# Optimization experiments

Hardware: AMD Instinct MI355X
Metric: run time of the kernel (lower is better)

## Reference

```python
import jax, jax.numpy as jnp
import numpy as np

B, L, I, O = 65536, 16, 256, 256


def setup_inputs() -> dict:
    key = jax.random.key(0)
    k1, k2, k3, k4 = jax.random.split(key, 4)
    lookups = jax.random.uniform(k1, (B, L), dtype=jnp.float32)
    values = jax.random.normal(k2, (B, I), dtype=jnp.float32)
    # glorot-style scale for the weight bank
    weights_lookup = jax.random.normal(k3, (L, I, O), dtype=jnp.float32) * (1.0 / np.sqrt(I))
    bias_lookup = jnp.zeros((L, O), dtype=jnp.float32)
    return {"lookups": lookups, "values": values,
            "weights_lookup": weights_lookup, "bias_lookup": bias_lookup}


def reference(lookups, values, weights_lookup, bias_lookup):
    # tf.einsum('...i,...l,lio->...o') with bias einsum('...l,lo->...o'),
    # activation = 'linear' (identity).
    # Efficient contraction order: per-token routed values (b,l,i) is avoided by
    # contracting values with the weight bank per expert, then combining with
    # routing weights — equivalent math, single einsum lets XLA pick the order.
    weighted = jnp.einsum('bi,bl,lio->bo', values, lookups, weights_lookup)
    biases = jnp.einsum('bl,lo->bo', lookups, bias_lookup)
    return weighted + biases
```

## Files before the change

kernel.cpp:

```cpp
#include <hip/hip_runtime.h>
#include <hip/hip_fp16.h>
#include <stdint.h>


#define B_TOK 65536
#define L_DIM 16
#define I_DIM 256
#define O_DIM 256
#define NKT   65
#define BM    256
#define BN    256
#define BK    64
#define THREADS 512

typedef __attribute__((ext_vector_type(8))) _Float16 f16x8;
typedef __attribute__((ext_vector_type(4))) float f32x4;

typedef __attribute__((address_space(3))) void      lds_void_t;
typedef const __attribute__((address_space(1))) void gbl_void_t;

__global__ void prep_w(const float* __restrict__ W, const float* __restrict__ bias,
                       unsigned short* __restrict__ ws) {
    const int t = blockIdx.x;
    const int o = threadIdx.x;
    char* dstRow = (char*)(ws + (size_t)t * 16384) + o * 128;
    if (t < 64) {
        const int l = t & 15, ibase = (t >> 4) * 64;
        const float* src = W + ((size_t)l * I_DIM + ibase) * O_DIM + o;
#pragma unroll
        for (int c = 0; c < 8; ++c) {
            uint32_t p[4];
#pragma unroll
            for (int jp = 0; jp < 4; ++jp) {
                float a = src[(size_t)(c * 8 + 2 * jp) * O_DIM];
                float b = src[(size_t)(c * 8 + 2 * jp + 1) * O_DIM];
                p[jp] = __builtin_bit_cast(uint32_t, __floats2half2_rn(a, b));
            }
            uint4 q = {p[0], p[1], p[2], p[3]};
            *(uint4*)(dstRow + ((c ^ (o & 7)) * 16)) = q;
        }
    } else {
#pragma unroll
        for (int c = 0; c < 8; ++c) {
            uint32_t p[4] = {0u, 0u, 0u, 0u};
            if (c < 2) {
#pragma unroll
                for (int jp = 0; jp < 4; ++jp) {
                    int kk = c * 8 + 2 * jp;
                    float a = bias[(size_t)kk * O_DIM + o];
                    float b = bias[(size_t)(kk + 1) * O_DIM + o];
                    p[jp] = __builtin_bit_cast(uint32_t, __floats2half2_rn(a, b));
                }
            }
            uint4 q = {p[0], p[1], p[2], p[3]};
            *(uint4*)(dstRow + ((c ^ (o & 7)) * 16)) = q;
        }
    }
}

__launch_bounds__(THREADS, 2)
__global__ void md_gemm(const float* __restrict__ lookups,
                        const float* __restrict__ values,
                        const unsigned short* __restrict__ Wst,
                        float* __restrict__ out) {
    __shared__ char smem[2 * 65536];

    const int tid  = threadIdx.x;
    const int wid  = tid >> 6;
    const int lane = tid & 63;
    const int row0 = blockIdx.x * BM;

    const int r = tid >> 1;
    const int h = tid & 1;

    const int wm   = wid >> 2;
    const int wn   = wid & 3;
    const int arow = wm * 128 + (lane & 15);
    const int bcol = wn * 64  + (lane & 15);
    const int kkl  = (lane >> 4) * 8;

    f32x4 acc[8][4];
#pragma unroll
    for (int m = 0; m < 8; ++m)
#pragma unroll
        for (int n = 0; n < 4; ++n) acc[m][n] = (f32x4){0.f, 0.f, 0.f, 0.f};

    __half2 hvv[16];

    auto stageB = [&](int kt, int nb) {
        const char* src = (const char*)Wst + (size_t)kt * 32768 + wid * 1024 + lane * 16;
        char* dst = smem + nb * 65536 + 32768 + wid * 1024;
#pragma unroll
        for (int s = 0; s < 4; ++s)
            __builtin_amdgcn_global_load_lds((gbl_void_t*)(src + s * 8192),
                                             (lds_void_t*)(dst + s * 8192), 16, 0, 0);
    };

    auto prepA = [&](int kt) {
        if (kt < 64) {
            if ((kt & 15) == 0) {
                const float4* vp = (const float4*)(values + (size_t)(row0 + r) * I_DIM
                                                   + (kt >> 4) * 64 + h * 32);
#pragma unroll
                for (int j = 0; j < 8; ++j) {
                    float4 f = vp[j];
                    hvv[2 * j]     = __floats2half2_rn(f.x, f.y);
                    hvv[2 * j + 1] = __floats2half2_rn(f.z, f.w);
                }
            }
        } else {
            if (h == 0) {
                const float4* lp = (const float4*)(lookups + (size_t)(row0 + r) * L_DIM);
#pragma unroll
                for (int j = 0; j < 4; ++j) {
                    float4 f = lp[j];
                    hvv[2 * j]     = __floats2half2_rn(f.x, f.y);
                    hvv[2 * j + 1] = __floats2half2_rn(f.z, f.w);
                }
#pragma unroll
                for (int j = 8; j < 16; ++j) hvv[j] = __floats2half2_rn(0.f, 0.f);
            } else {
#pragma unroll
                for (int j = 0; j < 16; ++j) hvv[j] = __floats2half2_rn(0.f, 0.f);
            }
        }
    };

    auto writeA = [&](int nb, float sc) {
        __half2 s2 = __float2half2_rn(sc);
        uint32_t p[16];
#pragma unroll
        for (int i = 0; i < 16; ++i)
            p[i] = __builtin_bit_cast(uint32_t, __hmul2(hvv[i], s2));
        char* abase = smem + nb * 65536;
#pragma unroll
        for (int w = 0; w < 4; ++w) {
            uint4 q = {p[4 * w], p[4 * w + 1], p[4 * w + 2], p[4 * w + 3]};
            *(uint4*)(abase + ((r * 128 + h * 64 + w * 16) ^ ((r & 7) << 4))) = q;
        }
    };

    auto compute = [&](int bs) {
        char* abase = smem + bs * 65536;
        char* bbase = abase + 32768;
#pragma unroll
        for (int ks = 0; ks < 2; ++ks) {
            const int kk2 = kkl * 2 + ks * 64;
            f16x8 af[8], bfr[4];
#pragma unroll
            for (int nt = 0; nt < 4; ++nt) {
                int o = bcol + nt * 16;
                bfr[nt] = *(f16x8*)(bbase + ((o * 128 + kk2) ^ ((o & 7) << 4)));
            }
#pragma unroll
            for (int mt = 0; mt < 8; ++mt) {
                int row = arow + mt * 16;
                af[mt] = *(f16x8*)(abase + ((row * 128 + kk2) ^ ((row & 7) << 4)));
            }
#pragma unroll
            for (int mt = 0; mt < 8; ++mt)
#pragma unroll
                for (int nt = 0; nt < 4; ++nt)
                    acc[mt][nt] = __builtin_amdgcn_mfma_f32_16x16x32_f16(
                        af[mt], bfr[nt], acc[mt][nt], 0, 0, 0);
        }
    };

    stageB(0, 0);
    prepA(0);
    {
        float lk0 = lookups[(size_t)(row0 + r) * L_DIM];
        writeA(0, lk0);
    }
    __syncthreads();

    int bsel = 0;
    for (int kt = 0; kt < NKT; ++kt) {
        float lkn = 0.f;
        if (kt + 1 < NKT) {
            stageB(kt + 1, bsel ^ 1);
            prepA(kt + 1);
            lkn = (kt + 1 < 64) ? lookups[(size_t)(row0 + r) * L_DIM + ((kt + 1) & 15)]
                                : 1.0f;
        }
        compute(bsel);
        if (kt + 1 < NKT) writeA(bsel ^ 1, lkn);
        __syncthreads();
        bsel ^= 1;
    }

    const int orow = row0 + wm * 128 + (lane >> 4) * 4;
    const int ocol = wn * 64 + (lane & 15);
#pragma unroll
    for (int mt = 0; mt < 8; ++mt)
#pragma unroll
        for (int nt = 0; nt < 4; ++nt) {
#pragma unroll
            for (int j = 0; j < 4; ++j)
                out[(size_t)(orow + mt * 16 + j) * O_DIM + ocol + nt * 16] = acc[mt][nt][j];
        }
}

extern "C" void kernel_launch(void* const* d_in, const int* in_sizes, int n_in,
                              void* d_out, int out_size, void* d_ws, size_t ws_size,
                              hipStream_t stream) {
    const float* lookups = (const float*)d_in[0];
    const float* values  = (const float*)d_in[1];
    const float* W       = (const float*)d_in[2];
    const float* bias    = (const float*)d_in[3];
    unsigned short* Wst  = (unsigned short*)d_ws;

    prep_w<<<dim3(NKT), dim3(256), 0, stream>>>(W, bias, Wst);
    md_gemm<<<dim3(B_TOK / BM), dim3(THREADS), 0, stream>>>(lookups, values, Wst,
                                                            (float*)d_out);
}
```

Baseline: 231.7 us.

## Keep values tile resident per chunk and scale by lookups in registers

The A (values) tile is now written to LDS once per 64-wide input chunk and reused across all 16 experts. Each expert's routing weight is applied to the A fragments in registers, with the lookups read from an LDS cache, instead of rewriting the scaled A tile to LDS on every k-step. B staging uses a separate double buffer synchronised with a raw waitcnt plus barrier, and the bias tile is handled as a final step. prep_w is also spread over more blocks so the weight conversion runs with more parallelism. The intent is to cut LDS writes, global lookup loads and sync overhead, at the cost of more hand-written synchronisation that could hide races.

```diff
diff --git a/kernel.cpp b/kernel.cpp
--- a/kernel.cpp
+++ b/kernel.cpp
@@ -7,55 +7,54 @@
 #define L_DIM 16
 #define I_DIM 256
 #define O_DIM 256
-#define NKT   65
 #define BM    256
-#define BN    256
-#define BK    64
 #define THREADS 512
+
+#define AOFF  65536
+#define LKOFF 98304
+#define LKS   20
 
 typedef __attribute__((ext_vector_type(8))) _Float16 f16x8;
 typedef __attribute__((ext_vector_type(4))) float f32x4;
-
 typedef __attribute__((address_space(3))) void      lds_void_t;
 typedef const __attribute__((address_space(1))) void gbl_void_t;
 
+static __device__ __forceinline__ f16x8 scale8(f16x8 a, __half2 s) {
+    union { f16x8 v; __half2 h[4]; } u; u.v = a;
+#pragma unroll
+    for (int q = 0; q < 4; ++q) u.h[q] = __hmul2(u.h[q], s);
+    return u.v;
+}
+
 __global__ void prep_w(const float* __restrict__ W, const float* __restrict__ bias,
                        unsigned short* __restrict__ ws) {
-    const int t = blockIdx.x;
-    const int o = threadIdx.x;
-    char* dstRow = (char*)(ws + (size_t)t * 16384) + o * 128;
+    const int t  = blockIdx.x;
+    const int o  = blockIdx.y * 32 + (threadIdx.x & 31);
+    const int cp = threadIdx.x >> 5;
+    const int c  = cp ^ (o & 7);
+    uint32_t p[4];
     if (t < 64) {
         const int l = t & 15, ibase = (t >> 4) * 64;
-        const float* src = W + ((size_t)l * I_DIM + ibase) * O_DIM + o;
-#pragma unroll
-        for (int c = 0; c < 8; ++c) {
-            uint32_t p[4];
-#pragma unroll
-            for (int jp = 0; jp < 4; ++jp) {
-                float a = src[(size_t)(c * 8 + 2 * jp) * O_DIM];
-                float b = src[(size_t)(c * 8 + 2 * jp + 1) * O_DIM];
-                p[jp] = __builtin_bit_cast(uint32_t, __floats2half2_rn(a, b));
-            }
-            uint4 q = {p[0], p[1], p[2], p[3]};
-            *(uint4*)(dstRow + ((c ^ (o & 7)) * 16)) = q;
+        const float* src = W + ((size_t)l * I_DIM + ibase + c * 8) * O_DIM + o;
+#pragma unroll
+        for (int jp = 0; jp < 4; ++jp) {
+            float a = src[(size_t)(2 * jp) * O_DIM];
+            float b = src[(size_t)(2 * jp + 1) * O_DIM];
+            p[jp] = __builtin_bit_cast(uint32_t, __floats2half2_rn(a, b));
+        }
+    } else if (c < 2) {
+#pragma unroll
+        for (int jp = 0; jp < 4; ++jp) {
+            int kk = c * 8 + 2 * jp;
+            float a = bias[(size_t)kk * O_DIM + o];
+            float b = bias[(size_t)(kk + 1) * O_DIM + o];
+            p[jp] = __builtin_bit_cast(uint32_t, __floats2half2_rn(a, b));
         }
     } else {
-#pragma unroll
-        for (int c = 0; c < 8; ++c) {
-            uint32_t p[4] = {0u, 0u, 0u, 0u};
-            if (c < 2) {
-#pragma unroll
-                for (int jp = 0; jp < 4; ++jp) {
-                    int kk = c * 8 + 2 * jp;
-                    float a = bias[(size_t)kk * O_DIM + o];
-                    float b = bias[(size_t)(kk + 1) * O_DIM + o];
-                    p[jp] = __builtin_bit_cast(uint32_t, __floats2half2_rn(a, b));
-                }
-            }
-            uint4 q = {p[0], p[1], p[2], p[3]};
-            *(uint4*)(dstRow + ((c ^ (o & 7)) * 16)) = q;
-        }
-    }
+        p[0] = p[1] = p[2] = p[3] = 0u;
+    }
+    uint4 q = {p[0], p[1], p[2], p[3]};
+    *(uint4*)((char*)ws + (size_t)t * 32768 + o * 128 + cp * 16) = q;
 }
 
 __launch_bounds__(THREADS, 2)
@@ -63,7 +62,7 @@
                         const float* __restrict__ values,
                         const unsigned short* __restrict__ Wst,
                         float* __restrict__ out) {
-    __shared__ char smem[2 * 65536];
+    __shared__ char smem[118784];
 
     const int tid  = threadIdx.x;
     const int wid  = tid >> 6;
@@ -85,108 +84,133 @@
 #pragma unroll
         for (int n = 0; n < 4; ++n) acc[m][n] = (f32x4){0.f, 0.f, 0.f, 0.f};
 
-    __half2 hvv[16];
-
     auto stageB = [&](int kt, int nb) {
         const char* src = (const char*)Wst + (size_t)kt * 32768 + wid * 1024 + lane * 16;
-        char* dst = smem + nb * 65536 + 32768 + wid * 1024;
+        char* dst = smem + nb * 32768 + wid * 1024;
 #pragma unroll
         for (int s = 0; s < 4; ++s)
             __builtin_amdgcn_global_load_lds((gbl_void_t*)(src + s * 8192),
                                              (lds_void_t*)(dst + s * 8192), 16, 0, 0);
     };
 
-    auto prepA = [&](int kt) {
-        if (kt < 64) {
-            if ((kt & 15) == 0) {
-                const float4* vp = (const float4*)(values + (size_t)(row0 + r) * I_DIM
-                                                   + (kt >> 4) * 64 + h * 32);
-#pragma unroll
-                for (int j = 0; j < 8; ++j) {
-                    float4 f = vp[j];
-                    hvv[2 * j]     = __floats2half2_rn(f.x, f.y);
-                    hvv[2 * j + 1] = __floats2half2_rn(f.z, f.w);
-                }
-            }
-        } else {
-            if (h == 0) {
-                const float4* lp = (const float4*)(lookups + (size_t)(row0 + r) * L_DIM);
-#pragma unroll
-                for (int j = 0; j < 4; ++j) {
-                    float4 f = lp[j];
-                    hvv[2 * j]     = __floats2half2_rn(f.x, f.y);
-                    hvv[2 * j + 1] = __floats2half2_rn(f.z, f.w);
-                }
-#pragma unroll
-                for (int j = 8; j < 16; ++j) hvv[j] = __floats2half2_rn(0.f, 0.f);
-            } else {
-#pragma unroll
-                for (int j = 0; j < 16; ++j) hvv[j] = __floats2half2_rn(0.f, 0.f);
-            }
-        }
-    };
-
-    auto writeA = [&](int nb, float sc) {
-        __half2 s2 = __float2half2_rn(sc);
+    {
+        const float4* lp = (const float4*)(lookups + (size_t)(row0 + r) * L_DIM + h * 8);
+        float4 f0 = lp[0], f1 = lp[1];
+        float* dst = (float*)(smem + LKOFF) + r * LKS + h * 8;
+        *(float4*)dst = f0;
+        *(float4*)(dst + 4) = f1;
+    }
+    stageB(0, 0);
+
+    const float* lkp = (const float*)(smem + LKOFF);
+
+    for (int cc = 0; cc < 4; ++cc) {
+        {
+            const float4* vp = (const float4*)(values + (size_t)(row0 + r) * I_DIM
+                                               + cc * 64 + h * 32);
+            uint32_t p[16];
+#pragma unroll
+            for (int j = 0; j < 8; ++j) {
+                float4 f = vp[j];
+                p[2 * j]     = __builtin_bit_cast(uint32_t, __floats2half2_rn(f.x, f.y));
+                p[2 * j + 1] = __builtin_bit_cast(uint32_t, __floats2half2_rn(f.z, f.w));
+            }
+            char* ab = smem + AOFF;
+#pragma unroll
+            for (int w = 0; w < 4; ++w) {
+                uint4 q = {p[4 * w], p[4 * w + 1], p[4 * w + 2], p[4 * w + 3]};
+                *(uint4*)(ab + ((r * 128 + h * 64 + w * 16) ^ ((r & 7) << 4))) = q;
+            }
+        }
+        __syncthreads();
+
+        f16x8 afk0[8];
+#pragma unroll
+        for (int mt = 0; mt < 8; ++mt) {
+            int row = arow + mt * 16;
+            afk0[mt] = *(f16x8*)(smem + AOFF + ((row * 128 + kkl * 2) ^ ((row & 7) << 4)));
+        }
+
+        for (int l = 0; l < 16; ++l) {
+            const int kt = cc * 16 + l;
+            if (l != 0) {
+                asm volatile("s_waitcnt vmcnt(0)\n\ts_barrier" ::: "memory");
+            }
+            __half2 lk2[8];
+#pragma unroll
+            for (int mt = 0; mt < 8; ++mt)
+                lk2[mt] = __float2half2_rn(lkp[(arow + mt * 16) * LKS + l]);
+
+            char* bbase = smem + (kt & 1) * 32768;
+            f16x8 bfr[4];
+#pragma unroll
+            for (int nt = 0; nt < 4; ++nt) {
+                int o = bcol + nt * 16;
+                bfr[nt] = *(f16x8*)(bbase + ((o * 128 + kkl * 2) ^ ((o & 7) << 4)));
+            }
+#pragma unroll
+            for (int mt = 0; mt < 8; ++mt) {
+                f16x8 a = scale8(afk0[mt], lk2[mt]);
+#pragma unroll
+                for (int nt = 0; nt < 4; ++nt)
+                    acc[mt][nt] = __builtin_amdgcn_mfma_f32_16x16x32_f16(
+                        a, bfr[nt], acc[mt][nt], 0, 0, 0);
+            }
+#pragma unroll
+            for (int nt = 0; nt < 4; ++nt) {
+                int o = bcol + nt * 16;
+                bfr[nt] = *(f16x8*)(bbase + ((o * 128 + 64 + kkl * 2) ^ ((o & 7) << 4)));
+            }
+#pragma unroll
+            for (int mt = 0; mt < 8; ++mt) {
+                int row = arow + mt * 16;
+                f16x8 a1 = *(f16x8*)(smem + AOFF
+                                     + ((row * 128 + 64 + kkl * 2) ^ ((row & 7) << 4)));
+                a1 = scale8(a1, lk2[mt]);
+#pragma unroll
+                for (int nt = 0; nt < 4; ++nt)
+                    acc[mt][nt] = __builtin_amdgcn_mfma_f32_16x16x32_f16(
+                        a1, bfr[nt], acc[mt][nt], 0, 0, 0);
+            }
+            stageB(kt + 1, (kt + 1) & 1);
+        }
+        asm volatile("s_barrier" ::: "memory");
+    }
+
+    {
         uint32_t p[16];
 #pragma unroll
-        for (int i = 0; i < 16; ++i)
-            p[i] = __builtin_bit_cast(uint32_t, __hmul2(hvv[i], s2));
-        char* abase = smem + nb * 65536;
+        for (int j = 0; j < 16; ++j) p[j] = 0u;
+        if (h == 0) {
+            const float* lr = lkp + r * LKS;
+#pragma unroll
+            for (int j = 0; j < 8; ++j)
+                p[j] = __builtin_bit_cast(uint32_t, __floats2half2_rn(lr[2 * j], lr[2 * j + 1]));
+        }
+        char* ab = smem + AOFF;
 #pragma unroll
         for (int w = 0; w < 4; ++w) {
             uint4 q = {p[4 * w], p[4 * w + 1], p[4 * w + 2], p[4 * w + 3]};
-            *(uint4*)(abase + ((r * 128 + h * 64 + w * 16) ^ ((r & 7) << 4))) = q;
-        }
-    };
-
-    auto compute = [&](int bs) {
-        char* abase = smem + bs * 65536;
-        char* bbase = abase + 32768;
-#pragma unroll
-        for (int ks = 0; ks < 2; ++ks) {
-            const int kk2 = kkl * 2 + ks * 64;
-            f16x8 af[8], bfr[4];
-#pragma unroll
-            for (int nt = 0; nt < 4; ++nt) {
-                int o = bcol + nt * 16;
-                bfr[nt] = *(f16x8*)(bbase + ((o * 128 + kk2) ^ ((o & 7) << 4)));
-            }
-#pragma unroll
-            for (int mt = 0; mt < 8; ++mt) {
-                int row = arow + mt * 16;
-                af[mt] = *(f16x8*)(abase + ((row * 128 + kk2) ^ ((row & 7) << 4)));
-            }
-#pragma unroll
-            for (int mt = 0; mt < 8; ++mt)
-#pragma unroll
-                for (int nt = 0; nt < 4; ++nt)
-                    acc[mt][nt] = __builtin_amdgcn_mfma_f32_16x16x32_f16(
-                        af[mt], bfr[nt], acc[mt][nt], 0, 0, 0);
-        }
-    };
-
-    stageB(0, 0);
-    prepA(0);
+            *(uint4*)(ab + ((r * 128 + h * 64 + w * 16) ^ ((r & 7) << 4))) = q;
+        }
+    }
+    __syncthreads();
     {
-        float lk0 = lookups[(size_t)(row0 + r) * L_DIM];
-        writeA(0, lk0);
-    }
-    __syncthreads();
-
-    int bsel = 0;
-    for (int kt = 0; kt < NKT; ++kt) {
-        float lkn = 0.f;
-        if (kt + 1 < NKT) {
-            stageB(kt + 1, bsel ^ 1);
-            prepA(kt + 1);
-            lkn = (kt + 1 < 64) ? lookups[(size_t)(row0 + r) * L_DIM + ((kt + 1) & 15)]
-                                : 1.0f;
-        }
-        compute(bsel);
-        if (kt + 1 < NKT) writeA(bsel ^ 1, lkn);
-        __syncthreads();
-        bsel ^= 1;
+        f16x8 bfr[4];
+#pragma unroll
+        for (int nt = 0; nt < 4; ++nt) {
+            int o = bcol + nt * 16;
+            bfr[nt] = *(f16x8*)(smem + ((o * 128 + kkl * 2) ^ ((o & 7) << 4)));
+        }
+#pragma unroll
+        for (int mt = 0; mt < 8; ++mt) {
+            int row = arow + mt * 16;
+            f16x8 a0 = *(f16x8*)(smem + AOFF + ((row * 128 + kkl * 2) ^ ((row & 7) << 4)));
+#pragma unroll
+            for (int nt = 0; nt < 4; ++nt)
+                acc[mt][nt] = __builtin_amdgcn_mfma_f32_16x16x32_f16(
+                    a0, bfr[nt], acc[mt][nt], 0, 0, 0);
+        }
     }
 
     const int orow = row0 + wm * 128 + (lane >> 4) * 4;
@@ -210,7 +234,7 @@
     const float* bias    = (const float*)d_in[3];
     unsigned short* Wst  = (unsigned short*)d_ws;
 
-    prep_w<<<dim3(NKT), dim3(256), 0, stream>>>(W, bias, Wst);
+    prep_w<<<dim3(65, 8), dim3(256), 0, stream>>>(W, bias, Wst);
     md_gemm<<<dim3(B_TOK / BM), dim3(THREADS), 0, stream>>>(lookups, values, Wst,
                                                             (float*)d_out);
 }
```

Measured after the change: 233.3 us. Within noise of the previous version (+0.7%).
